# Performance work log

Measured on AMD Instinct MI355X. Metric: run time of the kernel, lower is better.

The kernel has to match this reference:

```python
import jax, jax.numpy as jnp
import numpy as np
from jax import lax

EPS = 1e-6
S = 0.025  # EMA smoothing coefficient


def setup_inputs() -> dict:
    key = jax.random.key(0)
    x = jax.random.normal(key, (64, 1, 128, 8000), dtype=jnp.float32)
    log_alpha = jnp.array(-1.0, dtype=jnp.float32)
    log_delta = jnp.array(0.0, dtype=jnp.float32)
    log_r = jnp.array(-1.0, dtype=jnp.float32)
    return {"x": x, "log_alpha": log_alpha, "log_delta": log_delta, "log_r": log_r}


def reference(x, log_alpha, log_delta, log_r):
    alpha = jnp.clip(jnp.exp(log_alpha), 0.01, 1.0)
    delta = jnp.clip(jnp.exp(log_delta), 0.01, 5.0)
    r = jnp.clip(jnp.exp(log_r), 0.01, 1.0)

    xe = jnp.exp(x)[:, 0]           # [B, F, T] energy
    xt = jnp.moveaxis(xe, -1, 0)    # [T, B, F] for time scan

    def step(m, x_t):
        m = (1.0 - S) * m + S * x_t
        return m, m

    m0 = jnp.zeros(xe.shape[:-1], dtype=xe.dtype)  # [B, F]
    _, Ms = lax.scan(step, m0, xt)                 # [T, B, F]
    M = jnp.moveaxis(Ms, 0, -1)                    # [B, F, T]

    out = (xe / (EPS + M) ** alpha + delta) ** r - delta ** r
    return out[:, None]  # [B, 1, F, T]
```

## Files before the change

### kernel.cpp

```cpp
#include <hip/hip_runtime.h>

#define S_COEF 0.025f
#define EPS_C  1e-6f
#define L2E    1.4426950408889634f

typedef float f32x4 __attribute__((ext_vector_type(4)));

__device__ __forceinline__ float fexp2(float v) { return __builtin_amdgcn_exp2f(v); }
__device__ __forceinline__ float flog2(float v) { return __builtin_amdgcn_logf(v); }

__global__ __launch_bounds__(256) void pcen_kernel(
    const float* __restrict__ x,
    const float* __restrict__ p_la,
    const float* __restrict__ p_ld,
    const float* __restrict__ p_lr,
    float* __restrict__ out,
    int rows, int T)
{
    const int lane = threadIdx.x & 63;
    const int wid  = blockIdx.x * (blockDim.x >> 6) + (threadIdx.x >> 6);
    if (wid >= rows) return;

    const float alpha = fminf(fmaxf(__expf(p_la[0]), 0.01f), 1.0f);
    const float delta = fminf(fmaxf(__expf(p_ld[0]), 0.01f), 5.0f);
    const float r     = fminf(fmaxf(__expf(p_lr[0]), 0.01f), 1.0f);
    const float dr    = fexp2(r * flog2(delta));

    const float u     = 1.0f - S_COEF;
    const float u4    = u * u * u * u;
    const float uinv4 = 1.0f / u4;
    const float log2u = flog2(u);
    const float winv  = fexp2(-4.0f * (float)lane * log2u);
    const float ul4   = fexp2( 4.0f * (float)lane * log2u);

    const float* __restrict__ xr  = x   + (size_t)wid * T;
    float* __restrict__       orr = out + (size_t)wid * T;

    const int ngroups = (T + 255) >> 8;
    const int myoff   = lane * 4;
    float carry = 0.0f;

    f32x4 cur = (myoff < T) ? *(const f32x4*)(xr + myoff)
                            : (f32x4){0.f, 0.f, 0.f, 0.f};

    for (int g = 0; g < ngroups; ++g) {
        const int base = g << 8;
        const int nidx = base + 256 + myoff;
        f32x4 nxt = (nidx < T) ? *(const f32x4*)(xr + nidx)
                               : (f32x4){0.f, 0.f, 0.f, 0.f};

        const float xl0 = cur.x * L2E, xl1 = cur.y * L2E;
        const float xl2 = cur.z * L2E, xl3 = cur.w * L2E;
        const float e0 = fexp2(xl0), e1 = fexp2(xl1);
        const float e2 = fexp2(xl2), e3 = fexp2(xl3);

        const float se0 = S_COEF * e0, se1 = S_COEF * e1;
        const float se2 = S_COEF * e2, se3 = S_COEF * e3;

        float b = se0;
        b = fmaf(u, b, se1);
        b = fmaf(u, b, se2);
        b = fmaf(u, b, se3);

        const float scaled = b * winv;
        float ps = scaled;
        #pragma unroll
        for (int d = 1; d < 64; d <<= 1) {
            float n = __shfl_up(ps, d, 64);
            if (lane >= d) ps += n;
        }

        const float m_in = ul4 * fmaf(ps - scaled, uinv4, carry);

        const float m0 = fmaf(u, m_in, se0);
        const float m1 = fmaf(u, m0,   se1);
        const float m2 = fmaf(u, m1,   se2);
        const float m3 = fmaf(u, m2,   se3);

        carry = __shfl(m3, 63, 64);

        const float ed0 = fexp2(fmaf(-alpha, flog2(m0 + EPS_C), xl0));
        const float ed1 = fexp2(fmaf(-alpha, flog2(m1 + EPS_C), xl1));
        const float ed2 = fexp2(fmaf(-alpha, flog2(m2 + EPS_C), xl2));
        const float ed3 = fexp2(fmaf(-alpha, flog2(m3 + EPS_C), xl3));

        const float o0 = fexp2(r * flog2(ed0 + delta)) - dr;
        const float o1 = fexp2(r * flog2(ed1 + delta)) - dr;
        const float o2 = fexp2(r * flog2(ed2 + delta)) - dr;
        const float o3 = fexp2(r * flog2(ed3 + delta)) - dr;

        if (base + myoff < T) {
            f32x4 o4 = {o0, o1, o2, o3};
            __builtin_nontemporal_store(o4, (f32x4*)(orr + base + myoff));
        }
        cur = nxt;
    }
}

extern "C" void kernel_launch(void* const* d_in, const int* in_sizes, int n_in,
                              void* d_out, int out_size, void* d_ws, size_t ws_size,
                              hipStream_t stream) {
    const float* x  = (const float*)d_in[0];
    const float* la = (const float*)d_in[1];
    const float* ld = (const float*)d_in[2];
    const float* lr = (const float*)d_in[3];
    float* out = (float*)d_out;

    const int T    = 8000;
    const int rows = in_sizes[0] / T;
    const int wavesPerBlock = 4;
    const int blocks = (rows + wavesPerBlock - 1) / wavesPerBlock;

    hipLaunchKernelGGL(pcen_kernel, dim3(blocks), dim3(256), 0, stream,
                       x, la, ld, lr, out, rows, T);
}
```

Measured before the change: 85.94 us.

## Use DPP wave scan and process eight elements per lane in PCEN

Replaces the shuffle-based 64-lane prefix scan with a DPP row-shift and row-broadcast inclusive scan, and reads the carry with readlane. Each lane now handles eight consecutive elements per iteration, so a wave covers 512 time steps. This halves the number of cross-lane scans and loop iterations per row and lowers cross-lane communication latency. The cost is higher register pressure and wider decay-factor ranges in the scaled scan, which may lose some floating-point precision.

After: 102.2 us. +18.9%, slower.

```diff
diff --git a/kernel.cpp b/kernel.cpp
--- a/kernel.cpp
+++ b/kernel.cpp
@@ -8,6 +8,23 @@
 
 __device__ __forceinline__ float fexp2(float v) { return __builtin_amdgcn_exp2f(v); }
 __device__ __forceinline__ float flog2(float v) { return __builtin_amdgcn_logf(v); }
+
+template<int CTRL, int RM, bool BC>
+__device__ __forceinline__ float dpp_add(float v) {
+    int t = __builtin_amdgcn_update_dpp(0, __builtin_bit_cast(int, v),
+                                        CTRL, RM, 0xF, BC);
+    return v + __builtin_bit_cast(float, t);
+}
+
+__device__ __forceinline__ float wave_incl_scan(float v) {
+    v = dpp_add<0x111, 0xF, true >(v);
+    v = dpp_add<0x112, 0xF, true >(v);
+    v = dpp_add<0x114, 0xF, true >(v);
+    v = dpp_add<0x118, 0xF, true >(v);
+    v = dpp_add<0x142, 0xA, false>(v);
+    v = dpp_add<0x143, 0xC, false>(v);
+    return v;
+}
 
 __global__ __launch_bounds__(256) void pcen_kernel(
     const float* __restrict__ x,
@@ -27,73 +44,75 @@
     const float dr    = fexp2(r * flog2(delta));
 
     const float u     = 1.0f - S_COEF;
-    const float u4    = u * u * u * u;
-    const float uinv4 = 1.0f / u4;
     const float log2u = flog2(u);
-    const float winv  = fexp2(-4.0f * (float)lane * log2u);
-    const float ul4   = fexp2( 4.0f * (float)lane * log2u);
+    const float uinv8 = fexp2(-8.0f * log2u);
+    const float winv  = fexp2(-8.0f * (float)lane * log2u);
+    const float ul8   = fexp2( 8.0f * (float)lane * log2u);
 
     const float* __restrict__ xr  = x   + (size_t)wid * T;
     float* __restrict__       orr = out + (size_t)wid * T;
 
-    const int ngroups = (T + 255) >> 8;
-    const int myoff   = lane * 4;
+    const int ngroups = (T + 511) >> 9;
+    const int myoff   = lane * 8;
     float carry = 0.0f;
 
-    f32x4 cur = (myoff < T) ? *(const f32x4*)(xr + myoff)
-                            : (f32x4){0.f, 0.f, 0.f, 0.f};
+    f32x4 cur0 = {0.f,0.f,0.f,0.f}, cur1 = {0.f,0.f,0.f,0.f};
+    if (myoff < T) {
+        cur0 = *(const f32x4*)(xr + myoff);
+        cur1 = *(const f32x4*)(xr + myoff + 4);
+    }
 
     for (int g = 0; g < ngroups; ++g) {
-        const int base = g << 8;
-        const int nidx = base + 256 + myoff;
-        f32x4 nxt = (nidx < T) ? *(const f32x4*)(xr + nidx)
-                               : (f32x4){0.f, 0.f, 0.f, 0.f};
+        const int base = g << 9;
+        const int nidx = base + 512 + myoff;
+        f32x4 nxt0 = {0.f,0.f,0.f,0.f}, nxt1 = {0.f,0.f,0.f,0.f};
+        if (nidx < T) {
+            nxt0 = *(const f32x4*)(xr + nidx);
+            nxt1 = *(const f32x4*)(xr + nidx + 4);
+        }
 
-        const float xl0 = cur.x * L2E, xl1 = cur.y * L2E;
-        const float xl2 = cur.z * L2E, xl3 = cur.w * L2E;
-        const float e0 = fexp2(xl0), e1 = fexp2(xl1);
-        const float e2 = fexp2(xl2), e3 = fexp2(xl3);
+        float c[8] = {cur0.x, cur0.y, cur0.z, cur0.w,
+                      cur1.x, cur1.y, cur1.z, cur1.w};
+        float xl[8], se[8];
+        #pragma unroll
+        for (int i = 0; i < 8; ++i) {
+            xl[i] = c[i] * L2E;
+            se[i] = S_COEF * fexp2(xl[i]);
+        }
 
-        const float se0 = S_COEF * e0, se1 = S_COEF * e1;
-        const float se2 = S_COEF * e2, se3 = S_COEF * e3;
-
-        float b = se0;
-        b = fmaf(u, b, se1);
-        b = fmaf(u, b, se2);
-        b = fmaf(u, b, se3);
+        float b = se[0];
+        #pragma unroll
+        for (int i = 1; i < 8; ++i) b = fmaf(u, b, se[i]);
 
         const float scaled = b * winv;
-        float ps = scaled;
+        const float ps     = wave_incl_scan(scaled);
+        const float excl   = ps - scaled;
+
+        const float m_in = ul8 * fmaf(excl, uinv8, carry);
+
+        float m[8];
+        float mm = m_in;
         #pragma unroll
-        for (int d = 1; d < 64; d <<= 1) {
-            float n = __shfl_up(ps, d, 64);
-            if (lane >= d) ps += n;
+        for (int i = 0; i < 8; ++i) { mm = fmaf(u, mm, se[i]); m[i] = mm; }
+
+        carry = __builtin_bit_cast(float,
+                    __builtin_amdgcn_readlane(__builtin_bit_cast(int, m[7]), 63));
+
+        float o[8];
+        #pragma unroll
+        for (int i = 0; i < 8; ++i) {
+            const float ed = fexp2(fmaf(-alpha, flog2(m[i] + EPS_C), xl[i]));
+            o[i] = fexp2(r * flog2(ed + delta)) - dr;
         }
 
-        const float m_in = ul4 * fmaf(ps - scaled, uinv4, carry);
-
-        const float m0 = fmaf(u, m_in, se0);
-        const float m1 = fmaf(u, m0,   se1);
-        const float m2 = fmaf(u, m1,   se2);
-        const float m3 = fmaf(u, m2,   se3);
-
-        carry = __shfl(m3, 63, 64);
-
-        const float ed0 = fexp2(fmaf(-alpha, flog2(m0 + EPS_C), xl0));
-        const float ed1 = fexp2(fmaf(-alpha, flog2(m1 + EPS_C), xl1));
-        const float ed2 = fexp2(fmaf(-alpha, flog2(m2 + EPS_C), xl2));
-        const float ed3 = fexp2(fmaf(-alpha, flog2(m3 + EPS_C), xl3));
-
-        const float o0 = fexp2(r * flog2(ed0 + delta)) - dr;
-        const float o1 = fexp2(r * flog2(ed1 + delta)) - dr;
-        const float o2 = fexp2(r * flog2(ed2 + delta)) - dr;
-        const float o3 = fexp2(r * flog2(ed3 + delta)) - dr;
-
         if (base + myoff < T) {
-            f32x4 o4 = {o0, o1, o2, o3};
-            __builtin_nontemporal_store(o4, (f32x4*)(orr + base + myoff));
+            f32x4 o0 = {o[0], o[1], o[2], o[3]};
+            f32x4 o1 = {o[4], o[5], o[6], o[7]};
+            __builtin_nontemporal_store(o0, (f32x4*)(orr + base + myoff));
+            __builtin_nontemporal_store(o1, (f32x4*)(orr + base + myoff + 4));
         }
-        cur = nxt;
+        cur0 = nxt0;
+        cur1 = nxt1;
     }
 }
 
```
